# Kernel optimization log

Measured on AMD Instinct MI355X. Metric: run time of the kernel, lower is better.

## Reference

```python
import jax, jax.numpy as jnp
import numpy as np

E = 576        # embed_dims
HEADS = 18
NPTS = 12
NF = 3         # num_frames
DD = 2 * NF - 1  # depth of value volume (5)
HD = E // HEADS  # head dim (32)


def _grid_init_bias():
    # Faithful reproduction of init_weights() for sampling_offsets.bias
    theta = np.arange(8) * (2.0 * np.pi / 8)
    yaw = np.stack([np.cos(theta), np.sin(theta), np.zeros(8)], -1)
    roll = np.stack([np.zeros(8), np.cos(theta), np.sin(theta)], -1)
    pitch = np.stack([np.cos(theta), np.zeros(8), np.sin(theta)], -1)
    g = np.concatenate([yaw, pitch[[1, 2, 3, 5, 6, 7]], roll[[1, 3, 5, 7]]], 0)  # (18,3)
    g = g / np.abs(g).max(-1, keepdims=True)
    g = np.tile(g[:, None, None, :], (1, 1, NPTS, 1))              # (18,1,12,3)
    g = g * np.arange(1, NPTS + 1, dtype=np.float64)[None, None, :, None]
    return g.reshape(-1).astype(np.float32)                        # (18*12*3,)


def setup_inputs() -> dict:
    key = jax.random.key(0)
    ks = jax.random.split(key, 6)
    bs, h, w = 2, 64, 80
    nq = h * w
    lim = float(np.sqrt(6.0 / (E + E)))  # xavier uniform for square E x E
    return {
        "query": jax.random.normal(ks[0], (bs, nq, E), jnp.float32),
        "value": jax.random.normal(ks[1], (bs, nq * DD, E), jnp.float32),
        "query_pos": jax.random.normal(ks[2], (bs, nq, E), jnp.float32),
        "W_off": jnp.zeros((E, HEADS * NPTS * 3), jnp.float32),  # constant_init 0
        "b_off": jnp.asarray(_grid_init_bias()),
        "W_attn": jnp.zeros((E, HEADS * NPTS), jnp.float32),
        "b_attn": jnp.zeros((HEADS * NPTS,), jnp.float32),
        "W_v": jax.random.uniform(ks[3], (E, E), jnp.float32, -lim, lim),
        "b_v": jnp.zeros((E,), jnp.float32),
        "W_out": jax.random.uniform(ks[4], (E, E), jnp.float32, -lim, lim),
        "b_out": jnp.zeros((E,), jnp.float32),
        "h": 64,
        "w": 80,
    }


def _deform_attn_3d(value, loc, attn, D, H, W):
    # value: (bs, D*H*W, heads, hd)  token order: depth-major (D, H, W)
    # loc:   (bs, nq, heads, np, 3)  normalized (x, y, z) in [0,1]
    # attn:  (bs, nq, heads, np)
    bs, _, heads, hd = value.shape
    nq = loc.shape[1]
    # (bs, heads, D*H*W, hd) flat spatial for gathers
    v = value.reshape(bs, D, H, W, heads, hd).transpose(0, 4, 1, 2, 3, 5)
    v = v.reshape(bs, heads, D * H * W, hd)
    lt = jnp.moveaxis(loc, 2, 1)    # (bs, heads, nq, np, 3)
    at = jnp.moveaxis(attn, 2, 1)   # (bs, heads, nq, np)
    # grid_sample(align_corners=False) coordinate convention: pix = u*size - 0.5
    x = lt[..., 0] * W - 0.5
    y = lt[..., 1] * H - 0.5
    z = lt[..., 2] * D - 0.5
    x0 = jnp.floor(x); y0 = jnp.floor(y); z0 = jnp.floor(z)
    fx = x - x0; fy = y - y0; fz = z - z0
    acc = jnp.zeros((bs, heads, nq, NPTS, hd), v.dtype)
    for dz in (0, 1):
        for dy in (0, 1):
            for dx in (0, 1):
                xi = x0 + dx; yi = y0 + dy; zi = z0 + dz
                wgt = ((fx if dx else 1.0 - fx)
                       * (fy if dy else 1.0 - fy)
                       * (fz if dz else 1.0 - fz))
                valid = ((xi >= 0) & (xi < W) & (yi >= 0) & (yi < H)
                         & (zi >= 0) & (zi < D))
                xc = jnp.clip(xi, 0, W - 1).astype(jnp.int32)
                yc = jnp.clip(yi, 0, H - 1).astype(jnp.int32)
                zc = jnp.clip(zi, 0, D - 1).astype(jnp.int32)
                idx = ((zc * H + yc) * W + xc).reshape(bs, heads, nq * NPTS)
                g = jnp.take_along_axis(v, idx[..., None], axis=2)
                g = g.reshape(bs, heads, nq, NPTS, hd)
                acc = acc + g * (wgt * valid.astype(v.dtype))[..., None]
    out = jnp.einsum("bhqp,bhqpd->bhqd", at, acc)  # softmax-weighted sum over points
    return out.transpose(0, 2, 1, 3).reshape(bs, nq, heads * hd)


def _forward(query, value, query_pos, W_off, b_off, W_attn, b_attn,
             W_v, b_v, W_out, b_out, h, w):
    bs, nq, _ = query.shape
    q = query + query_pos
    v = (value @ W_v + b_v).reshape(bs, nq * DD, HEADS, HD)
    offs = (q @ W_off + b_off).reshape(bs, nq, HEADS, NPTS, 3)
    attn = jax.nn.softmax((q @ W_attn + b_attn).reshape(bs, nq, HEADS, NPTS), axis=-1)
    # reference points: pixel centers normalized, z = 0
    ry, rx = jnp.meshgrid((jnp.arange(h, dtype=jnp.float32) + 0.5) / h,
                          (jnp.arange(w, dtype=jnp.float32) + 0.5) / w,
                          indexing="ij")
    ref = jnp.stack([rx.reshape(-1), ry.reshape(-1),
                     jnp.zeros(h * w, jnp.float32)], -1)  # (nq, 3)
    norm = jnp.array([w, h, NF], jnp.float32)  # NOTE: z normalized by num_frames (as in source)
    loc = ref[None, :, None, None, :] + offs / norm
    out = _deform_attn_3d(v, loc, attn, DD, h, w)
    return out @ W_out + b_out  # dropout is identity at eval


def reference(query, value, query_pos, W_off, b_off, W_attn, b_attn,
              W_v, b_v, W_out, b_out, h, w):
    return _forward(query, value, query_pos, W_off, b_off, W_attn, b_attn,
                    W_v, b_v, W_out, b_out, h, w)
```

## Files before the change

kernel.cpp:

```cpp
#include <hip/hip_runtime.h>
#include <cstdint>

#define E_DIM   576
#define HEADS   18
#define NPTS    12
#define DDEPTH  5
#define HDIM    32
#define BSZ     2
#define GH      64
#define GW      80
#define NQ      (GH*GW)
#define NTOK    (NQ*DDEPTH)
#define MIXW    864
#define BQ_TOT  (BSZ*NQ)

typedef __attribute__((ext_vector_type(8))) short short8;
typedef __attribute__((ext_vector_type(4))) float f32x4;

__device__ __forceinline__ float b2f_lo(uint32_t u) {
    union { uint32_t u; float f; } v; v.u = u << 16; return v.f;
}
__device__ __forceinline__ float b2f_hi(uint32_t u) {
    union { uint32_t u; float f; } v; v.u = u & 0xffff0000u; return v.f;
}
__device__ __forceinline__ ushort f2b(float f) {
    union { float f; uint32_t u; } v; v.f = f;
    return (ushort)((v.u + 0x7fffu + ((v.u >> 16) & 1u)) >> 16);
}

__global__ void cast_kernel(const float* __restrict__ in, ushort* __restrict__ out, int n4) {
    int i = blockIdx.x * blockDim.x + threadIdx.x;
    if (i >= n4) return;
    const float4 v = reinterpret_cast<const float4*>(in)[i];
    ushort4 o; o.x = f2b(v.x); o.y = f2b(v.y); o.z = f2b(v.z); o.w = f2b(v.w);
    reinterpret_cast<ushort4*>(out)[i] = o;
}

__global__ void cast_add_kernel(const float* __restrict__ a, const float* __restrict__ b,
                                ushort* __restrict__ out, int n4) {
    int i = blockIdx.x * blockDim.x + threadIdx.x;
    if (i >= n4) return;
    const float4 va = reinterpret_cast<const float4*>(a)[i];
    const float4 vb = reinterpret_cast<const float4*>(b)[i];
    ushort4 o;
    o.x = f2b(va.x + vb.x); o.y = f2b(va.y + vb.y);
    o.z = f2b(va.z + vb.z); o.w = f2b(va.w + vb.w);
    reinterpret_cast<ushort4*>(out)[i] = o;
}

__global__ void prep_weights(const float* __restrict__ W_v, const float* __restrict__ W_out,
                             const float* __restrict__ W_off, const float* __restrict__ W_attn,
                             const float* __restrict__ b_off, const float* __restrict__ b_attn,
                             ushort* __restrict__ wt_v, ushort* __restrict__ wt_out,
                             ushort* __restrict__ wt_mix, float* __restrict__ bias_mix) {
    int idx = blockIdx.x * blockDim.x + threadIdx.x;
    if (idx < 864) bias_mix[idx] = (idx < 648) ? b_off[idx] : b_attn[idx - 648];
    if (idx < 331776) {
        int n = idx / E_DIM, k = idx - n * E_DIM;
        wt_v[idx] = f2b(W_v[(size_t)k * E_DIM + n]);
    } else if (idx < 663552) {
        int j = idx - 331776;
        int n = j / E_DIM, k = j - n * E_DIM;
        wt_out[j] = f2b(W_out[(size_t)k * E_DIM + n]);
    } else if (idx < 1161216) {
        int j = idx - 663552;
        int n = j / E_DIM, k = j - n * E_DIM;
        float v = (n < 648) ? W_off[(size_t)k * 648 + n] : W_attn[(size_t)k * 216 + (n - 648)];
        wt_mix[j] = f2b(v);
    }
}

#define TM 128
#define TN 96
#define BK 32

__device__ __forceinline__ void async_cp16(const ushort* gsrc, ushort* ldst) {
    __builtin_amdgcn_global_load_lds(
        (const __attribute__((address_space(1))) void*)gsrc,
        (__attribute__((address_space(3))) void*)ldst, 16, 0, 0);
}

template <typename OutT>
__global__ void gemm_mfma(const ushort* __restrict__ A, const ushort* __restrict__ Bt,
                          const float* __restrict__ bias, OutT* __restrict__ C,
                          int M, int N, int K, int ldc) {
    __shared__ __align__(16) ushort Asb[TM * BK];
    __shared__ __align__(16) ushort Bsb[TN * BK];
    const int tid  = threadIdx.x;
    const int wave = tid >> 6;
    const int lane = tid & 63;
    const int m16  = lane & 15;
    const int quad = lane >> 4;
    const int wr   = wave >> 1;
    const int wc   = wave & 1;
    const int row0 = blockIdx.x * TM;
    const int n0   = blockIdx.y * TN;

    const f32x4 zero = {0.f, 0.f, 0.f, 0.f};
    f32x4 acc[4][3];
    #pragma unroll
    for (int rt = 0; rt < 4; ++rt)
        #pragma unroll
        for (int ct = 0; ct < 3; ++ct) acc[rt][ct] = zero;

    const int srow = lane >> 2;
    const int scol = (((lane & 3) ^ ((lane >> 3) & 3))) * 8;
    const int ksw  = (quad ^ ((m16 >> 1) & 3)) * 8;

    for (int k0 = 0; k0 < K; k0 += BK) {
        #pragma unroll
        for (int c = 0; c < 2; ++c) {
            const int ch = wave + c * 4;
            async_cp16(A + (size_t)(row0 + ch * 16 + srow) * K + k0 + scol,
                       Asb + ch * 512 + lane * 8);
        }
        {
            const int ch = wave;
            if (ch < 6)
                async_cp16(Bt + (size_t)(n0 + ch * 16 + srow) * K + k0 + scol,
                           Bsb + ch * 512 + lane * 8);
            const int ch2 = wave + 4;
            if (ch2 < 6)
                async_cp16(Bt + (size_t)(n0 + ch2 * 16 + srow) * K + k0 + scol,
                           Bsb + ch2 * 512 + lane * 8);
        }
        __syncthreads();

        short8 afrag[4], bfrag[3];
        #pragma unroll
        for (int rt = 0; rt < 4; ++rt)
            afrag[rt] = *reinterpret_cast<const short8*>(
                Asb + (wr * 4 + rt) * 512 + m16 * 32 + ksw);
        #pragma unroll
        for (int ct = 0; ct < 3; ++ct)
            bfrag[ct] = *reinterpret_cast<const short8*>(
                Bsb + (wc * 3 + ct) * 512 + m16 * 32 + ksw);

        #pragma unroll
        for (int rt = 0; rt < 4; ++rt)
            #pragma unroll
            for (int ct = 0; ct < 3; ++ct)
                acc[rt][ct] = __builtin_amdgcn_mfma_f32_16x16x32_bf16(
                    afrag[rt], bfrag[ct], acc[rt][ct], 0, 0, 0);

        __syncthreads();
    }

    #pragma unroll
    for (int ct = 0; ct < 3; ++ct) {
        const int col = n0 + wc * 48 + ct * 16 + m16;
        const float bcol = bias[col];
        #pragma unroll
        for (int rt = 0; rt < 4; ++rt) {
            #pragma unroll
            for (int r = 0; r < 4; ++r) {
                const int row = row0 + wr * 64 + rt * 16 + quad * 4 + r;
                const float val = acc[rt][ct][r] + bcol;
                if constexpr (__is_same(OutT, float)) {
                    C[(size_t)row * ldc + col] = val;
                } else {
                    C[(size_t)row * ldc + col] = f2b(val);
                }
            }
        }
    }
}

__global__ void __launch_bounds__(256, 8)
deform_kernel(const ushort* __restrict__ vbuf,
              const float* __restrict__ mix,
              ushort* __restrict__ aout) {
    const int gl   = threadIdx.x >> 4;
    const int l    = threadIdx.x & 15;
    const int head = blockIdx.x / 640;
    const int bq   = (blockIdx.x % 640) * 16 + gl;
    const int q    = bq % NQ;
    const int b    = bq / NQ;
    const int qx   = q % GW;
    const int qy   = q / GW;

    const float* mrow = mix + (size_t)bq * MIXW;

    float lg = (l < NPTS) ? mrow[648 + head * NPTS + l] : -1e30f;
    float mx = lg;
    #pragma unroll
    for (int mk = 1; mk < 16; mk <<= 1) mx = fmaxf(mx, __shfl_xor(mx, mk, 16));
    float e = (l < NPTS) ? __expf(lg - mx) : 0.f;
    float s = e;
    #pragma unroll
    for (int mk = 1; mk < 16; mk <<= 1) s += __shfl_xor(s, mk, 16);

    float    cw[8];
    uint32_t coff[8];
    uint32_t mask = 0;
    {
        const float ap = e / s;
        const int pl = (l < NPTS) ? l : 0;
        const int ob = (head * NPTS + pl) * 3;
        const float ox = mrow[ob + 0];
        const float oy = mrow[ob + 1];
        const float oz = mrow[ob + 2];
        const float x = (float)qx + ox;
        const float y = (float)qy + oy;
        const float z = oz * (5.0f / 3.0f) - 0.5f;
        const float x0f = floorf(x), y0f = floorf(y), z0f = floorf(z);
        const int x0 = (int)x0f, y0 = (int)y0f, z0 = (int)z0f;
        const float fx = x - x0f, fy = y - y0f, fz = z - z0f;

        #pragma unroll
        for (int dz = 0; dz < 2; ++dz) {
            const int zi = z0 + dz;
            const bool zv = (zi >= 0) & (zi < DDEPTH);
            const int zc = min(max(zi, 0), DDEPTH - 1);
            const float wz = dz ? fz : 1.f - fz;
            #pragma unroll
            for (int dy = 0; dy < 2; ++dy) {
                const int yi = y0 + dy;
                const bool yv = (yi >= 0) & (yi < GH);
                const int yc = min(max(yi, 0), GH - 1);
                const float wy = dy ? fy : 1.f - fy;
                #pragma unroll
                for (int dx = 0; dx < 2; ++dx) {
                    const int xi = x0 + dx;
                    const bool xv = (xi >= 0) & (xi < GW);
                    const int xc = min(max(xi, 0), GW - 1);
                    const float wx = dx ? fx : 1.f - fx;
                    const int i = dz * 4 + dy * 2 + dx;
                    const bool valid = zv & yv & xv & (l < NPTS);
                    cw[i]   = ap * wz * wy * wx;
                    coff[i] = (uint32_t)((zc * GH + yc) * GW + xc) * (E_DIM / 2);
                    mask |= (valid ? (1u << i) : 0u);
                }
            }
        }
    }

    const uint32_t* vb = reinterpret_cast<const uint32_t*>(vbuf)
                         + (size_t)b * NTOK * (E_DIM / 2) + head * (HDIM / 2) + l;
    float o0 = 0.f, o1 = 0.f;
    #pragma unroll
    for (int p = 0; p < NPTS; ++p) {
        const uint32_t msk = (uint32_t)__shfl((int)mask, p, 16);
        if (msk == 0) continue;
        #pragma unroll
        for (int i = 0; i < 8; ++i) {
            if (msk & (1u << i)) {
                const float    w   = __shfl(cw[i], p, 16);
                const uint32_t off = (uint32_t)__shfl((int)coff[i], p, 16);
                const uint32_t pair = vb[off];
                o0 += w * b2f_lo(pair);
                o1 += w * b2f_hi(pair);
            }
        }
    }
    const uint32_t packed = (uint32_t)f2b(o0) | ((uint32_t)f2b(o1) << 16);
    reinterpret_cast<uint32_t*>(aout)[(size_t)bq * (E_DIM / 2) + head * (HDIM / 2) + l] = packed;
}

extern "C" void kernel_launch(void* const* d_in, const int* in_sizes, int n_in,
                              void* d_out, int out_size, void* d_ws, size_t ws_size,
                              hipStream_t stream) {
    const float* query     = (const float*)d_in[0];
    const float* value     = (const float*)d_in[1];
    const float* query_pos = (const float*)d_in[2];
    const float* W_off     = (const float*)d_in[3];
    const float* b_off     = (const float*)d_in[4];
    const float* W_attn    = (const float*)d_in[5];
    const float* b_attn    = (const float*)d_in[6];
    const float* W_v       = (const float*)d_in[7];
    const float* b_v       = (const float*)d_in[8];
    const float* W_out     = (const float*)d_in[9];
    const float* b_out     = (const float*)d_in[10];
    float* out = (float*)d_out;

    char* ws = (char*)d_ws;
    ushort* vbuf     = (ushort*)(ws);
    ushort* val_bf16 = (ushort*)(ws + 58982400);
    ushort* aout     = val_bf16;
    ushort* q_bf16   = (ushort*)(ws + 117964800);
    float*  mixb     = (float*) (ws + 129761280);
    ushort* wt_v     = (ushort*)(ws + 165150720);
    ushort* wt_out   = (ushort*)(ws + 165814272);
    ushort* wt_mix   = (ushort*)(ws + 166477824);
    float*  bias_mix = (float*) (ws + 167473152);

    cast_kernel<<<(51200 * 576 / 4 + 255) / 256, 256, 0, stream>>>(value, val_bf16, 51200 * 576 / 4);
    cast_add_kernel<<<(10240 * 576 / 4 + 255) / 256, 256, 0, stream>>>(query, query_pos, q_bf16, 10240 * 576 / 4);
    prep_weights<<<(1161216 + 255) / 256, 256, 0, stream>>>(
        W_v, W_out, W_off, W_attn, b_off, b_attn, wt_v, wt_out, wt_mix, bias_mix);

    gemm_mfma<float><<<dim3(10240 / TM, MIXW / TN), 256, 0, stream>>>(
        q_bf16, wt_mix, bias_mix, mixb, BSZ * NQ, MIXW, E_DIM, MIXW);

    gemm_mfma<ushort><<<dim3(51200 / TM, E_DIM / TN), 256, 0, stream>>>(
        val_bf16, wt_v, b_v, vbuf, BSZ * NTOK, E_DIM, E_DIM, E_DIM);

    deform_kernel<<<HEADS * 640, 256, 0, stream>>>(vbuf, mixb, aout);

    gemm_mfma<float><<<dim3(10240 / TM, E_DIM / TN), 256, 0, stream>>>(
        aout, wt_out, b_out, out, BSZ * NQ, E_DIM, E_DIM, E_DIM);
}
```

Measured before the change: 401.7 us.

## Double-buffer LDS tiles in MFMA GEMM to overlap global loads with compute

Splits the A and B shared-memory tiles into two buffers and issues the async global-to-LDS copy for the next K step before computing on the current one, leaving one barrier per iteration. The aim is to hide global load latency behind the MFMA work. It doubles LDS use, which may lower occupancy. Correctness depends on the async loads being complete at the barrier; the code adds no explicit vmcnt wait, so there is a risk of reading stale tiles if the compiler does not insert one.

```diff
diff --git a/kernel.cpp b/kernel.cpp
--- a/kernel.cpp
+++ b/kernel.cpp
@@ -84,8 +84,8 @@
 __global__ void gemm_mfma(const ushort* __restrict__ A, const ushort* __restrict__ Bt,
                           const float* __restrict__ bias, OutT* __restrict__ C,
                           int M, int N, int K, int ldc) {
-    __shared__ __align__(16) ushort Asb[TM * BK];
-    __shared__ __align__(16) ushort Bsb[TN * BK];
+    __shared__ __align__(16) ushort Asb[2][TM * BK];
+    __shared__ __align__(16) ushort Bsb[2][TN * BK];
     const int tid  = threadIdx.x;
     const int wave = tid >> 6;
     const int lane = tid & 63;
@@ -107,34 +107,36 @@
     const int scol = (((lane & 3) ^ ((lane >> 3) & 3))) * 8;
     const int ksw  = (quad ^ ((m16 >> 1) & 3)) * 8;
 
-    for (int k0 = 0; k0 < K; k0 += BK) {
+    auto stage = [&](int buf, int k0) {
         #pragma unroll
         for (int c = 0; c < 2; ++c) {
             const int ch = wave + c * 4;
             async_cp16(A + (size_t)(row0 + ch * 16 + srow) * K + k0 + scol,
-                       Asb + ch * 512 + lane * 8);
+                       &Asb[buf][ch * 512 + lane * 8]);
         }
-        {
-            const int ch = wave;
-            if (ch < 6)
-                async_cp16(Bt + (size_t)(n0 + ch * 16 + srow) * K + k0 + scol,
-                           Bsb + ch * 512 + lane * 8);
-            const int ch2 = wave + 4;
-            if (ch2 < 6)
-                async_cp16(Bt + (size_t)(n0 + ch2 * 16 + srow) * K + k0 + scol,
-                           Bsb + ch2 * 512 + lane * 8);
-        }
-        __syncthreads();
+        async_cp16(Bt + (size_t)(n0 + wave * 16 + srow) * K + k0 + scol,
+                   &Bsb[buf][wave * 512 + lane * 8]);
+        if (wave < 2)
+            async_cp16(Bt + (size_t)(n0 + (wave + 4) * 16 + srow) * K + k0 + scol,
+                       &Bsb[buf][(wave + 4) * 512 + lane * 8]);
+    };
+
+    stage(0, 0);
+    __syncthreads();
+
+    int cur = 0;
+    for (int k0 = 0; k0 < K; k0 += BK) {
+        if (k0 + BK < K) stage(cur ^ 1, k0 + BK);
 
         short8 afrag[4], bfrag[3];
         #pragma unroll
         for (int rt = 0; rt < 4; ++rt)
             afrag[rt] = *reinterpret_cast<const short8*>(
-                Asb + (wr * 4 + rt) * 512 + m16 * 32 + ksw);
+                &Asb[cur][(wr * 4 + rt) * 512 + m16 * 32 + ksw]);
         #pragma unroll
         for (int ct = 0; ct < 3; ++ct)
             bfrag[ct] = *reinterpret_cast<const short8*>(
-                Bsb + (wc * 3 + ct) * 512 + m16 * 32 + ksw);
+                &Bsb[cur][(wc * 3 + ct) * 512 + m16 * 32 + ksw]);
 
         #pragma unroll
         for (int rt = 0; rt < 4; ++rt)
@@ -144,6 +146,7 @@
                     afrag[rt], bfrag[ct], acc[rt][ct], 0, 0, 0);
 
         __syncthreads();
+        cur ^= 1;
     }
 
     #pragma unroll
```

Result: no change. 398.0 us (-0.9%).

## Merge prep kernels, fuse the two projection GEMMs, stage deform corners in LDS

Applied to the files above, without the earlier changes.

The three cast/prep kernels become one launch, and the query-mix GEMM and value-projection GEMM now run as a single dual-dispatch launch split by block index. This removes launch gaps and lets the smaller GEMM's blocks fill the GPU alongside the larger one. The deform kernel now writes per-point corner weights, offsets and masks to shared memory behind a block barrier, replacing many cross-lane shuffles with LDS reads. The trade-off is extra shared memory and a __syncthreads, with a non-unrolled point loop, in a kernel launched with __launch_bounds__(256, 8).

```diff
diff --git a/kernel.cpp b/kernel.cpp
--- a/kernel.cpp
+++ b/kernel.cpp
@@ -28,42 +28,38 @@
     return (ushort)((v.u + 0x7fffu + ((v.u >> 16) & 1u)) >> 16);
 }
 
-__global__ void cast_kernel(const float* __restrict__ in, ushort* __restrict__ out, int n4) {
-    int i = blockIdx.x * blockDim.x + threadIdx.x;
-    if (i >= n4) return;
-    const float4 v = reinterpret_cast<const float4*>(in)[i];
-    ushort4 o; o.x = f2b(v.x); o.y = f2b(v.y); o.z = f2b(v.z); o.w = f2b(v.w);
-    reinterpret_cast<ushort4*>(out)[i] = o;
-}
-
-__global__ void cast_add_kernel(const float* __restrict__ a, const float* __restrict__ b,
-                                ushort* __restrict__ out, int n4) {
-    int i = blockIdx.x * blockDim.x + threadIdx.x;
-    if (i >= n4) return;
-    const float4 va = reinterpret_cast<const float4*>(a)[i];
-    const float4 vb = reinterpret_cast<const float4*>(b)[i];
-    ushort4 o;
-    o.x = f2b(va.x + vb.x); o.y = f2b(va.y + vb.y);
-    o.z = f2b(va.z + vb.z); o.w = f2b(va.w + vb.w);
-    reinterpret_cast<ushort4*>(out)[i] = o;
-}
-
-__global__ void prep_weights(const float* __restrict__ W_v, const float* __restrict__ W_out,
-                             const float* __restrict__ W_off, const float* __restrict__ W_attn,
-                             const float* __restrict__ b_off, const float* __restrict__ b_attn,
-                             ushort* __restrict__ wt_v, ushort* __restrict__ wt_out,
-                             ushort* __restrict__ wt_mix, float* __restrict__ bias_mix) {
-    int idx = blockIdx.x * blockDim.x + threadIdx.x;
-    if (idx < 864) bias_mix[idx] = (idx < 648) ? b_off[idx] : b_attn[idx - 648];
-    if (idx < 331776) {
-        int n = idx / E_DIM, k = idx - n * E_DIM;
-        wt_v[idx] = f2b(W_v[(size_t)k * E_DIM + n]);
-    } else if (idx < 663552) {
-        int j = idx - 331776;
+__global__ void prep_all(const float* __restrict__ value,
+                         const float* __restrict__ query, const float* __restrict__ query_pos,
+                         const float* __restrict__ W_v, const float* __restrict__ W_out,
+                         const float* __restrict__ W_off, const float* __restrict__ W_attn,
+                         const float* __restrict__ b_off, const float* __restrict__ b_attn,
+                         ushort* __restrict__ val_bf16, ushort* __restrict__ q_bf16,
+                         ushort* __restrict__ wt_v, ushort* __restrict__ wt_out,
+                         ushort* __restrict__ wt_mix, float* __restrict__ bias_mix) {
+    const int i = blockIdx.x * blockDim.x + threadIdx.x;
+    if (i < 51200 * 576 / 4) {
+        const float4 v = reinterpret_cast<const float4*>(value)[i];
+        ushort4 o; o.x = f2b(v.x); o.y = f2b(v.y); o.z = f2b(v.z); o.w = f2b(v.w);
+        reinterpret_cast<ushort4*>(val_bf16)[i] = o;
+    }
+    if (i < 10240 * 576 / 4) {
+        const float4 va = reinterpret_cast<const float4*>(query)[i];
+        const float4 vb = reinterpret_cast<const float4*>(query_pos)[i];
+        ushort4 o;
+        o.x = f2b(va.x + vb.x); o.y = f2b(va.y + vb.y);
+        o.z = f2b(va.z + vb.z); o.w = f2b(va.w + vb.w);
+        reinterpret_cast<ushort4*>(q_bf16)[i] = o;
+    }
+    if (i < 864) bias_mix[i] = (i < 648) ? b_off[i] : b_attn[i - 648];
+    if (i < 331776) {
+        int n = i / E_DIM, k = i - n * E_DIM;
+        wt_v[i] = f2b(W_v[(size_t)k * E_DIM + n]);
+    } else if (i < 663552) {
+        int j = i - 331776;
         int n = j / E_DIM, k = j - n * E_DIM;
         wt_out[j] = f2b(W_out[(size_t)k * E_DIM + n]);
-    } else if (idx < 1161216) {
-        int j = idx - 663552;
+    } else if (i < 1161216) {
+        int j = i - 663552;
         int n = j / E_DIM, k = j - n * E_DIM;
         float v = (n < 648) ? W_off[(size_t)k * 648 + n] : W_attn[(size_t)k * 216 + (n - 648)];
         wt_mix[j] = f2b(v);
@@ -81,11 +77,13 @@
 }
 
 template <typename OutT>
-__global__ void gemm_mfma(const ushort* __restrict__ A, const ushort* __restrict__ Bt,
-                          const float* __restrict__ bias, OutT* __restrict__ C,
-                          int M, int N, int K, int ldc) {
-    __shared__ __align__(16) ushort Asb[TM * BK];
-    __shared__ __align__(16) ushort Bsb[TN * BK];
+__device__ __forceinline__ void gemm_body(ushort* __restrict__ smem, int bx, int by,
+                                          const ushort* __restrict__ A,
+                                          const ushort* __restrict__ Bt,
+                                          const float* __restrict__ bias,
+                                          OutT* __restrict__ C, int K, int ldc) {
+    ushort* Asb = smem;
+    ushort* Bsb = smem + TM * BK;
     const int tid  = threadIdx.x;
     const int wave = tid >> 6;
     const int lane = tid & 63;
@@ -93,8 +91,8 @@
     const int quad = lane >> 4;
     const int wr   = wave >> 1;
     const int wc   = wave & 1;
-    const int row0 = blockIdx.x * TM;
-    const int n0   = blockIdx.y * TN;
+    const int row0 = bx * TM;
+    const int n0   = by * TN;
 
     const f32x4 zero = {0.f, 0.f, 0.f, 0.f};
     f32x4 acc[4][3];
@@ -114,16 +112,11 @@
             async_cp16(A + (size_t)(row0 + ch * 16 + srow) * K + k0 + scol,
                        Asb + ch * 512 + lane * 8);
         }
-        {
-            const int ch = wave;
-            if (ch < 6)
-                async_cp16(Bt + (size_t)(n0 + ch * 16 + srow) * K + k0 + scol,
-                           Bsb + ch * 512 + lane * 8);
-            const int ch2 = wave + 4;
-            if (ch2 < 6)
-                async_cp16(Bt + (size_t)(n0 + ch2 * 16 + srow) * K + k0 + scol,
-                           Bsb + ch2 * 512 + lane * 8);
-        }
+        async_cp16(Bt + (size_t)(n0 + wave * 16 + srow) * K + k0 + scol,
+                   Bsb + wave * 512 + lane * 8);
+        if (wave < 2)
+            async_cp16(Bt + (size_t)(n0 + (wave + 4) * 16 + srow) * K + k0 + scol,
+                       Bsb + (wave + 4) * 512 + lane * 8);
         __syncthreads();
 
         short8 afrag[4], bfrag[3];
@@ -166,10 +159,36 @@
     }
 }
 
+template <typename OutT>
+__global__ void gemm_mfma(const ushort* __restrict__ A, const ushort* __restrict__ Bt,
+                          const float* __restrict__ bias, OutT* __restrict__ C,
+                          int K, int ldc) {
+    __shared__ __align__(16) ushort smem[(TM + TN) * BK];
+    gemm_body<OutT>(smem, blockIdx.x, blockIdx.y, A, Bt, bias, C, K, ldc);
+}
+
+__global__ void gemm_dual(const ushort* __restrict__ A1, const ushort* __restrict__ B1,
+                          const float* __restrict__ bias1, float* __restrict__ C1,
+                          int K1, int ldc1, int nbx1, int split,
+                          const ushort* __restrict__ A2, const ushort* __restrict__ B2,
+                          const float* __restrict__ bias2, ushort* __restrict__ C2,
+                          int K2, int ldc2, int nbx2) {
+    __shared__ __align__(16) ushort smem[(TM + TN) * BK];
+    const int id = blockIdx.x;
+    if (id < split) {
+        gemm_body<float>(smem, id % nbx1, id / nbx1, A1, B1, bias1, C1, K1, ldc1);
+    } else {
+        const int j = id - split;
+        gemm_body<ushort>(smem, j % nbx2, j / nbx2, A2, B2, bias2, C2, K2, ldc2);
+    }
+}
+
 __global__ void __launch_bounds__(256, 8)
 deform_kernel(const ushort* __restrict__ vbuf,
               const float* __restrict__ mix,
               ushort* __restrict__ aout) {
+    __shared__ uint2 corn[16 * NPTS * 8];
+    __shared__ uint32_t cmask[16 * NPTS];
     const int gl   = threadIdx.x >> 4;
     const int l    = threadIdx.x & 15;
     const int head = blockIdx.x / 640;
@@ -235,19 +254,32 @@
         }
     }
 
+    if (l < NPTS) {
+        cmask[gl * NPTS + l] = mask;
+        uint4* dst = reinterpret_cast<uint4*>(&corn[(gl * NPTS + l) * 8]);
+        #pragma unroll
+        for (int i2 = 0; i2 < 4; ++i2) {
+            uint4 w;
+            w.x = __float_as_uint(cw[2 * i2]);     w.y = coff[2 * i2];
+            w.z = __float_as_uint(cw[2 * i2 + 1]); w.w = coff[2 * i2 + 1];
+            dst[i2] = w;
+        }
+    }
+    __syncthreads();
+
     const uint32_t* vb = reinterpret_cast<const uint32_t*>(vbuf)
                          + (size_t)b * NTOK * (E_DIM / 2) + head * (HDIM / 2) + l;
+    const uint2* cg = &corn[gl * NPTS * 8];
     float o0 = 0.f, o1 = 0.f;
-    #pragma unroll
     for (int p = 0; p < NPTS; ++p) {
-        const uint32_t msk = (uint32_t)__shfl((int)mask, p, 16);
+        const uint32_t msk = cmask[gl * NPTS + p];
         if (msk == 0) continue;
         #pragma unroll
         for (int i = 0; i < 8; ++i) {
             if (msk & (1u << i)) {
-                const float    w   = __shfl(cw[i], p, 16);
-                const uint32_t off = (uint32_t)__shfl((int)coff[i], p, 16);
-                const uint32_t pair = vb[off];
+                const uint2 wo = cg[p * 8 + i];
+                const float w = __uint_as_float(wo.x);
+                const uint32_t pair = vb[wo.y];
                 o0 += w * b2f_lo(pair);
                 o1 += w * b2f_hi(pair);
             }
@@ -284,19 +316,16 @@
     ushort* wt_mix   = (ushort*)(ws + 166477824);
     float*  bias_mix = (float*) (ws + 167473152);
 
-    cast_kernel<<<(51200 * 576 / 4 + 255) / 256, 256, 0, stream>>>(value, val_bf16, 51200 * 576 / 4);
-    cast_add_kernel<<<(10240 * 576 / 4 + 255) / 256, 256, 0, stream>>>(query, query_pos, q_bf16, 10240 * 576 / 4);
-    prep_weights<<<(1161216 + 255) / 256, 256, 0, stream>>>(
-        W_v, W_out, W_off, W_attn, b_off, b_attn, wt_v, wt_out, wt_mix, bias_mix);
-
-    gemm_mfma<float><<<dim3(10240 / TM, MIXW / TN), 256, 0, stream>>>(
-        q_bf16, wt_mix, bias_mix, mixb, BSZ * NQ, MIXW, E_DIM, MIXW);
-
-    gemm_mfma<ushort><<<dim3(51200 / TM, E_DIM / TN), 256, 0, stream>>>(
-        val_bf16, wt_v, b_v, vbuf, BSZ * NTOK, E_DIM, E_DIM, E_DIM);
+    prep_all<<<(51200 * 576 / 4) / 256, 256, 0, stream>>>(
+        value, query, query_pos, W_v, W_out, W_off, W_attn, b_off, b_attn,
+        val_bf16, q_bf16, wt_v, wt_out, wt_mix, bias_mix);
+
+    gemm_dual<<<720 + 2400, 256, 0, stream>>>(
+        q_bf16, wt_mix, bias_mix, mixb, E_DIM, MIXW, BQ_TOT / TM, 720,
+        val_bf16, wt_v, b_v, vbuf, E_DIM, E_DIM, (BSZ * NTOK) / TM);
 
     deform_kernel<<<HEADS * 640, 256, 0, stream>>>(vbuf, mixb, aout);
 
-    gemm_mfma<float><<<dim3(10240 / TM, E_DIM / TN), 256, 0, stream>>>(
-        aout, wt_out, b_out, out, BSZ * NQ, E_DIM, E_DIM, E_DIM);
-}
+    gemm_mfma<float><<<dim3(BQ_TOT / TM, E_DIM / TN), 256, 0, stream>>>(
+        aout, wt_out, b_out, out, E_DIM, E_DIM);
+}
```

After: 396.1 us. No clear change (-1.4%).
